# Kernel tuning notes

Hardware: AMD Instinct MI355X
Metric: run time of the kernel (lower is better)

## Reference

```python
import jax, jax.numpy as jnp
import numpy as np

B, S, E, H = 2, 2048, 512, 8
HD = E // H  # head dim = 64


def setup_inputs() -> dict:
    key = jax.random.key(0)
    k1, k2, k3 = jax.random.split(key, 3)
    scale_qkv = (6.0 / (E + 3 * E)) ** 0.5  # xavier-uniform-like scale
    scale_o = (6.0 / (E + E)) ** 0.5
    return {
        "X": jax.random.normal(k1, (B, S, E), dtype=jnp.float32),
        "Wqkv": jax.random.uniform(k2, (E, 3 * E), jnp.float32, -scale_qkv, scale_qkv),
        "bqkv": jnp.zeros((3 * E,), jnp.float32),
        "Wo": jax.random.uniform(k3, (E, E), jnp.float32, -scale_o, scale_o),
        "bo": jnp.zeros((E,), jnp.float32),
    }


def reference(X, Wqkv, bqkv, Wo, bo):
    b, s, e = X.shape
    # qkv projection: [B,S,3E] -> [B,S,H,3*HD] -> [B,H,S,3*HD]
    qkv = X @ Wqkv + bqkv
    qkv = qkv.reshape(b, s, H, 3 * HD).transpose(0, 2, 1, 3)
    q, k, v = jnp.array_split(qkv, 3, axis=-1)  # each [B,H,S,HD]
    # naive scaled dot-product attention (full score matrix, per source)
    attn_logits = jnp.einsum("bhqd,bhkd->bhqk", q, k) / jnp.sqrt(jnp.float32(HD))
    attention = jax.nn.softmax(attn_logits, axis=-1)  # [B,H,S,S]
    values = jnp.einsum("bhqk,bhkd->bhqd", attention, v)
    values = values.transpose(0, 2, 1, 3).reshape(b, s, e)
    o = values @ Wo + bo
    return (o, attention)
```

## Files before the change

### kernel.cpp

```cpp
#include <hip/hip_runtime.h>

typedef unsigned short u16;
typedef u16 u16x2 __attribute__((ext_vector_type(2)));
typedef u16 u16x4 __attribute__((ext_vector_type(4)));
typedef u16 u16x8 __attribute__((ext_vector_type(8)));
typedef __bf16 bf16x8 __attribute__((ext_vector_type(8)));
typedef float f32x4 __attribute__((ext_vector_type(4)));
typedef float f32x2 __attribute__((ext_vector_type(2)));

#define MFMA16(A, B, C) __builtin_amdgcn_mfma_f32_16x16x32_bf16(A, B, C, 0, 0, 0)

#define SB 2
#define SS 2048
#define SE 512
#define SH 8
#define SHD 64

__device__ __forceinline__ u16 f2b(float f) {
  union { float f; unsigned u; } v;
  v.f = f;
  unsigned r = v.u + 0x7FFFu + ((v.u >> 16) & 1u);
  return (u16)(r >> 16);
}

__device__ __forceinline__ bf16x8 as_bf16x8(u16x8 v) {
  return __builtin_bit_cast(bf16x8, v);
}

__global__ __launch_bounds__(256)
void prep_kernel(const float* __restrict__ X, u16* __restrict__ Xb,
                 const float* __restrict__ Wqkv, u16* __restrict__ WqkvT)
{
  __shared__ float t[32][33];
  const int tid = threadIdx.x;
  if (blockIdx.x < 2048) {
    const int i = (blockIdx.x * 256 + tid) * 4;
    const float4 v = *(const float4*)&X[i];
    u16x4 o;
    o[0] = f2b(v.x); o[1] = f2b(v.y); o[2] = f2b(v.z); o[3] = f2b(v.w);
    *(u16x4*)&Xb[i] = o;
  } else {
    const int bx = blockIdx.x - 2048;
    const int n0 = (bx % 48) * 32, k0 = (bx / 48) * 32;
    const int r = tid >> 3, c4 = (tid & 7) * 4;
    const float4 v = *(const float4*)&Wqkv[(size_t)(k0 + r) * 1536 + n0 + c4];
    t[r][c4 + 0] = v.x; t[r][c4 + 1] = v.y; t[r][c4 + 2] = v.z; t[r][c4 + 3] = v.w;
    __syncthreads();
    u16x4 o;
    o[0] = f2b(t[c4 + 0][r]);
    o[1] = f2b(t[c4 + 1][r]);
    o[2] = f2b(t[c4 + 2][r]);
    o[3] = f2b(t[c4 + 3][r]);
    *(u16x4*)&WqkvT[(n0 + r) * 512 + k0 + c4] = o;
  }
}

__global__ __launch_bounds__(256)
void wtrans_kernel(const float* __restrict__ in, u16* __restrict__ out, int N)
{
  __shared__ float t[32][33];
  const int tid = threadIdx.x;
  const int r = tid >> 3, c4 = (tid & 7) * 4;
  const int k0 = blockIdx.y * 32, n0 = blockIdx.x * 32;
  const float4 v = *(const float4*)&in[(size_t)(k0 + r) * N + n0 + c4];
  t[r][c4 + 0] = v.x; t[r][c4 + 1] = v.y; t[r][c4 + 2] = v.z; t[r][c4 + 3] = v.w;
  __syncthreads();
  u16x4 o;
  o[0] = f2b(t[c4 + 0][r]);
  o[1] = f2b(t[c4 + 1][r]);
  o[2] = f2b(t[c4 + 2][r]);
  o[3] = f2b(t[c4 + 3][r]);
  *(u16x4*)&out[(n0 + r) * 512 + k0 + c4] = o;
}

template <int MODE>
__global__ __launch_bounds__(256, 2)
void gemm_kernel(const u16* __restrict__ A, const u16* __restrict__ Bt,
                 const float* __restrict__ bias,
                 u16* __restrict__ Q, u16* __restrict__ K, u16* __restrict__ Vt,
                 float* __restrict__ Out)
{
  __shared__ __align__(16) u16 As[128 * 40];
  __shared__ __align__(16) u16 Bs[128 * 40];
  const int tid  = threadIdx.x;
  const int lane = tid & 63, wave = tid >> 6, quad = lane >> 4, l16 = lane & 15;
  const int m0 = blockIdx.y * 128, n0 = blockIdx.x * 128;
  const int wr = (wave >> 1) * 64, wc = (wave & 1) * 64;
  const int sr = tid >> 2, sc = (tid & 3) * 8;

  const f32x4 z4 = {0.f, 0.f, 0.f, 0.f};
  f32x4 acc[4][4];
#pragma unroll
  for (int i = 0; i < 4; i++)
#pragma unroll
    for (int j = 0; j < 4; j++) acc[i][j] = z4;

  for (int k0 = 0; k0 < 512; k0 += 32) {
    const u16x8 a0 = *(const u16x8*)&A[(m0 + sr) * 512 + k0 + sc];
    const u16x8 a1 = *(const u16x8*)&A[(m0 + 64 + sr) * 512 + k0 + sc];
    const u16x8 b0 = *(const u16x8*)&Bt[(n0 + sr) * 512 + k0 + sc];
    const u16x8 b1 = *(const u16x8*)&Bt[(n0 + 64 + sr) * 512 + k0 + sc];
    __syncthreads();
    *(u16x8*)&As[sr * 40 + sc]        = a0;
    *(u16x8*)&As[(64 + sr) * 40 + sc] = a1;
    *(u16x8*)&Bs[sr * 40 + sc]        = b0;
    *(u16x8*)&Bs[(64 + sr) * 40 + sc] = b1;
    __syncthreads();
    bf16x8 af[4], bf[4];
#pragma unroll
    for (int i = 0; i < 4; i++) {
      af[i] = as_bf16x8(*(const u16x8*)&As[(wr + i * 16 + l16) * 40 + quad * 8]);
      bf[i] = as_bf16x8(*(const u16x8*)&Bs[(wc + i * 16 + l16) * 40 + quad * 8]);
    }
#pragma unroll
    for (int i = 0; i < 4; i++)
#pragma unroll
      for (int j = 0; j < 4; j++) acc[i][j] = MFMA16(af[i], bf[j], acc[i][j]);
  }

#pragma unroll
  for (int tm = 0; tm < 4; tm++) {
#pragma unroll
    for (int tn = 0; tn < 4; tn++) {
#pragma unroll
      for (int r = 0; r < 4; r++) {
        const int gm = m0 + wr + tm * 16 + quad * 4 + r;
        const int gn = n0 + wc + tn * 16 + l16;
        const float v = acc[tm][tn][r] + bias[gn];
        if (MODE == 0) {
          const int bb = gm >> 11, s = gm & 2047;
          const int hh = gn / 192, j = gn - hh * 192;
          const int bh = bb * SH + hh;
          if (j < 64)
            Q[(bh * SS + s) * SHD + j] = f2b(v * 0.125f);
          else if (j < 128)
            K[(bh * SS + s) * SHD + (j - 64)] = f2b(v);
          else
            Vt[(bh * SHD + (j - 128)) * SS + s] = f2b(v);
        } else {
          Out[gm * 512 + gn] = v;
        }
      }
    }
  }
}

#define PSTR 264
#define PWAVE (16 * PSTR)

__global__ __launch_bounds__(512, 4)
void attn_kernel(const u16* __restrict__ Q, const u16* __restrict__ K,
                 const u16* __restrict__ Vt, u16* __restrict__ values,
                 float* __restrict__ attn)
{
  __shared__ __align__(16) u16 p_lds[8 * PWAVE];
  __shared__ float srm[8][16];
  __shared__ float srl[8][16];

  const int tid  = threadIdx.x;
  const int lane = tid & 63, wave = tid >> 6, quad = lane >> 4, l16 = lane & 15;
  const int q0 = blockIdx.x * 16;
  const int h = blockIdx.y, b = blockIdx.z, bh = b * SH + h;

  const u16* Qb = Q + (size_t)bh * SS * SHD;
  const u16* Kb = K + (size_t)bh * SS * SHD;
  const u16* Vb = Vt + (size_t)bh * SHD * SS;

  const bf16x8 aq0 = as_bf16x8(*(const u16x8*)&Qb[(q0 + l16) * SHD + quad * 8]);
  const bf16x8 aq1 = as_bf16x8(*(const u16x8*)&Qb[(q0 + l16) * SHD + 32 + quad * 8]);

  f32x4 acc[16];
#pragma unroll
  for (int ct = 0; ct < 16; ct++) {
    const int kb = wave * 256 + ct * 16;
    bf16x8 bk0 = as_bf16x8(*(const u16x8*)&Kb[(kb + l16) * SHD + quad * 8]);
    bf16x8 bk1 = as_bf16x8(*(const u16x8*)&Kb[(kb + l16) * SHD + 32 + quad * 8]);
    f32x4 c = {0.f, 0.f, 0.f, 0.f};
    c = MFMA16(aq0, bk0, c);
    c = MFMA16(aq1, bk1, c);
    acc[ct] = c;
  }

  float mw[4], lw[4];
#pragma unroll
  for (int r = 0; r < 4; r++) {
    float m = acc[0][r];
#pragma unroll
    for (int ct = 1; ct < 16; ct++) m = fmaxf(m, acc[ct][r]);
#pragma unroll
    for (int off = 1; off < 16; off <<= 1) m = fmaxf(m, __shfl_xor(m, off));
    mw[r] = m;
  }
#pragma unroll
  for (int r = 0; r < 4; r++) {
    float s = 0.f;
#pragma unroll
    for (int ct = 0; ct < 16; ct++) {
      const float p = __expf(acc[ct][r] - mw[r]);
      acc[ct][r] = p;
      s += p;
    }
#pragma unroll
    for (int off = 1; off < 16; off <<= 1) s += __shfl_xor(s, off);
    lw[r] = s;
  }
  if (l16 == 0) {
#pragma unroll
    for (int r = 0; r < 4; r++) {
      srm[wave][quad * 4 + r] = mw[r];
      srl[wave][quad * 4 + r] = lw[r];
    }
  }
  __syncthreads();

  float scale[4];
#pragma unroll
  for (int r = 0; r < 4; r++) {
    const int row = quad * 4 + r;
    float mg = srm[0][row];
#pragma unroll
    for (int w = 1; w < 8; w++) mg = fmaxf(mg, srm[w][row]);
    float lg = 0.f;
#pragma unroll
    for (int w = 0; w < 8; w++) lg += srl[w][row] * __expf(srm[w][row] - mg);
    scale[r] = __expf(mw[r] - mg) / lg;
  }
#pragma unroll
  for (int ct = 0; ct < 16; ct++)
#pragma unroll
    for (int r = 0; r < 4; r++) acc[ct][r] *= scale[r];

  u16* pl = &p_lds[wave * PWAVE];
#pragma unroll
  for (int ct = 0; ct < 16; ct++)
#pragma unroll
    for (int r = 0; r < 4; r++)
      pl[(quad * 4 + r) * PSTR + ct * 16 + l16] = f2b(acc[ct][r]);

  f32x4 oacc[4];
#pragma unroll
  for (int nt = 0; nt < 4; nt++) oacc[nt] = (f32x4){0.f, 0.f, 0.f, 0.f};
  bf16x8 vbuf[2][4];
  {
    const int sb = wave * 256 + quad * 8;
#pragma unroll
    for (int nt = 0; nt < 4; nt++)
      vbuf[0][nt] = as_bf16x8(*(const u16x8*)&Vb[(nt * 16 + l16) * SS + sb]);
  }
#pragma unroll
  for (int kc = 0; kc < 8; kc++) {
    if (kc < 7) {
      const int sb = wave * 256 + (kc + 1) * 32 + quad * 8;
#pragma unroll
      for (int nt = 0; nt < 4; nt++)
        vbuf[(kc + 1) & 1][nt] =
            as_bf16x8(*(const u16x8*)&Vb[(nt * 16 + l16) * SS + sb]);
    }
    bf16x8 pa = as_bf16x8(*(const u16x8*)&pl[l16 * PSTR + kc * 32 + quad * 8]);
#pragma unroll
    for (int nt = 0; nt < 4; nt++)
      oacc[nt] = MFMA16(pa, vbuf[kc & 1][nt], oacc[nt]);
  }

  float* op = (float*)pl;
#pragma unroll
  for (int nt = 0; nt < 4; nt++)
#pragma unroll
    for (int r = 0; r < 4; r++)
      op[(quad * 4 + r) * 64 + nt * 16 + l16] = oacc[nt][r];
  __syncthreads();

  const int q = tid >> 5, d0 = (tid & 31) * 2;
  f32x2 s2 = {0.f, 0.f};
#pragma unroll
  for (int w = 0; w < 8; w++) {
    const float* opw = (const float*)&p_lds[w * PWAVE];
    s2 += *(const f32x2*)&opw[q * 64 + d0];
  }
  u16x2 o2;
  o2[0] = f2b(s2[0]);
  o2[1] = f2b(s2[1]);
  *(u16x2*)&values[((size_t)(b * SS + q0 + q) * SH + h) * SHD + d0] = o2;

  float* attn_b = attn + ((size_t)bh * SS + q0) * SS;
#pragma unroll
  for (int ct = 0; ct < 16; ct++) {
    const int col = wave * 256 + ct * 16 + l16;
#pragma unroll
    for (int r = 0; r < 4; r++)
      __builtin_nontemporal_store(acc[ct][r], &attn_b[(quad * 4 + r) * SS + col]);
  }
}

extern "C" void kernel_launch(void* const* d_in, const int* in_sizes, int n_in,
                              void* d_out, int out_size, void* d_ws, size_t ws_size,
                              hipStream_t stream) {
  const float* X    = (const float*)d_in[0];
  const float* Wqkv = (const float*)d_in[1];
  const float* bqkv = (const float*)d_in[2];
  const float* Wo   = (const float*)d_in[3];
  const float* bo   = (const float*)d_in[4];

  float* o_out    = (float*)d_out;
  float* attn_out = o_out + SB * SS * SE;

  const size_t QKV_ELEMS = (size_t)SB * SH * SS * SHD;
  u16* Q      = (u16*)d_ws;
  u16* K      = Q + QKV_ELEMS;
  u16* Vt     = K + QKV_ELEMS;
  u16* values = Vt + QKV_ELEMS;
  u16* Xb     = values;
  u16* WqkvT  = (u16*)attn_out;
  u16* WoT    = Q;

  prep_kernel<<<dim3(2816), 256, 0, stream>>>(X, Xb, Wqkv, WqkvT);

  gemm_kernel<0><<<dim3(12, 32), 256, 0, stream>>>(Xb, WqkvT, bqkv, Q, K, Vt, nullptr);
  attn_kernel<<<dim3(128, 8, 2), 512, 0, stream>>>(Q, K, Vt, values, attn_out);
  wtrans_kernel<<<dim3(16, 16), 256, 0, stream>>>(Wo, WoT, 512);
  gemm_kernel<1><<<dim3(4, 32), 256, 0, stream>>>(values, WoT, bo,
                                                  nullptr, nullptr, nullptr, o_out);
}
```

Measured before the change: 421.3 us.

## Transpose MFMA operands so each lane owns one query row for vector stores

Swaps the A/B operands of the QK^T and PV MFMAs so the accumulator layout is transposed: each lane holds four consecutive key columns of a single query row. Row max and sum reductions become in-register work plus two cross-quad shuffles instead of four 16-lane shuffle trees. The attention-probability store to global memory becomes a 16-byte vector nontemporal store rather than four scalar stores, and the P and O LDS writes become vector stores, with a padded stride for O. The float-to-bf16 conversion now uses the compiler's native cast instead of manual rounding.

After: 436.8 us. 1.04x slower.

```diff
diff --git a/kernel.cpp b/kernel.cpp
--- a/kernel.cpp
+++ b/kernel.cpp
@@ -17,10 +17,7 @@
 #define SHD 64
 
 __device__ __forceinline__ u16 f2b(float f) {
-  union { float f; unsigned u; } v;
-  v.f = f;
-  unsigned r = v.u + 0x7FFFu + ((v.u >> 16) & 1u);
-  return (u16)(r >> 16);
+  return __builtin_bit_cast(u16, (__bf16)f);
 }
 
 __device__ __forceinline__ bf16x8 as_bf16x8(u16x8 v) {
@@ -147,6 +144,7 @@
 
 #define PSTR 264
 #define PWAVE (16 * PSTR)
+#define OSTR 72
 
 __global__ __launch_bounds__(512, 4)
 void attn_kernel(const u16* __restrict__ Q, const u16* __restrict__ K,
@@ -176,66 +174,59 @@
     bf16x8 bk0 = as_bf16x8(*(const u16x8*)&Kb[(kb + l16) * SHD + quad * 8]);
     bf16x8 bk1 = as_bf16x8(*(const u16x8*)&Kb[(kb + l16) * SHD + 32 + quad * 8]);
     f32x4 c = {0.f, 0.f, 0.f, 0.f};
-    c = MFMA16(aq0, bk0, c);
-    c = MFMA16(aq1, bk1, c);
+    c = MFMA16(bk0, aq0, c);
+    c = MFMA16(bk1, aq1, c);
     acc[ct] = c;
   }
 
-  float mw[4], lw[4];
-#pragma unroll
-  for (int r = 0; r < 4; r++) {
-    float m = acc[0][r];
-#pragma unroll
-    for (int ct = 1; ct < 16; ct++) m = fmaxf(m, acc[ct][r]);
-#pragma unroll
-    for (int off = 1; off < 16; off <<= 1) m = fmaxf(m, __shfl_xor(m, off));
-    mw[r] = m;
-  }
-#pragma unroll
-  for (int r = 0; r < 4; r++) {
-    float s = 0.f;
-#pragma unroll
-    for (int ct = 0; ct < 16; ct++) {
-      const float p = __expf(acc[ct][r] - mw[r]);
+  f32x4 mx4 = acc[0];
+#pragma unroll
+  for (int ct = 1; ct < 16; ct++)
+#pragma unroll
+    for (int r = 0; r < 4; r++) mx4[r] = fmaxf(mx4[r], acc[ct][r]);
+  float m = fmaxf(fmaxf(mx4[0], mx4[1]), fmaxf(mx4[2], mx4[3]));
+  m = fmaxf(m, __shfl_xor(m, 16));
+  m = fmaxf(m, __shfl_xor(m, 32));
+
+  f32x4 s4 = {0.f, 0.f, 0.f, 0.f};
+#pragma unroll
+  for (int ct = 0; ct < 16; ct++)
+#pragma unroll
+    for (int r = 0; r < 4; r++) {
+      const float p = __expf(acc[ct][r] - m);
       acc[ct][r] = p;
-      s += p;
+      s4[r] += p;
     }
-#pragma unroll
-    for (int off = 1; off < 16; off <<= 1) s += __shfl_xor(s, off);
-    lw[r] = s;
-  }
-  if (l16 == 0) {
-#pragma unroll
-    for (int r = 0; r < 4; r++) {
-      srm[wave][quad * 4 + r] = mw[r];
-      srl[wave][quad * 4 + r] = lw[r];
-    }
+  float s = (s4[0] + s4[1]) + (s4[2] + s4[3]);
+  s += __shfl_xor(s, 16);
+  s += __shfl_xor(s, 32);
+
+  if (lane < 16) {
+    srm[wave][l16] = m;
+    srl[wave][l16] = s;
   }
   __syncthreads();
 
-  float scale[4];
-#pragma unroll
-  for (int r = 0; r < 4; r++) {
-    const int row = quad * 4 + r;
-    float mg = srm[0][row];
-#pragma unroll
-    for (int w = 1; w < 8; w++) mg = fmaxf(mg, srm[w][row]);
-    float lg = 0.f;
-#pragma unroll
-    for (int w = 0; w < 8; w++) lg += srl[w][row] * __expf(srm[w][row] - mg);
-    scale[r] = __expf(mw[r] - mg) / lg;
-  }
+  float mg = srm[0][l16];
+#pragma unroll
+  for (int w = 1; w < 8; w++) mg = fmaxf(mg, srm[w][l16]);
+  float lg = 0.f;
+#pragma unroll
+  for (int w = 0; w < 8; w++) lg += srl[w][l16] * __expf(srm[w][l16] - mg);
+  const float scale = __expf(m - mg) / lg;
 #pragma unroll
   for (int ct = 0; ct < 16; ct++)
 #pragma unroll
-    for (int r = 0; r < 4; r++) acc[ct][r] *= scale[r];
+    for (int r = 0; r < 4; r++) acc[ct][r] *= scale;
 
   u16* pl = &p_lds[wave * PWAVE];
 #pragma unroll
-  for (int ct = 0; ct < 16; ct++)
-#pragma unroll
-    for (int r = 0; r < 4; r++)
-      pl[(quad * 4 + r) * PSTR + ct * 16 + l16] = f2b(acc[ct][r]);
+  for (int ct = 0; ct < 16; ct++) {
+    u16x4 t;
+#pragma unroll
+    for (int r = 0; r < 4; r++) t[r] = f2b(acc[ct][r]);
+    *(u16x4*)&pl[l16 * PSTR + ct * 16 + quad * 4] = t;
+  }
 
   f32x4 oacc[4];
 #pragma unroll
@@ -259,15 +250,13 @@
     bf16x8 pa = as_bf16x8(*(const u16x8*)&pl[l16 * PSTR + kc * 32 + quad * 8]);
 #pragma unroll
     for (int nt = 0; nt < 4; nt++)
-      oacc[nt] = MFMA16(pa, vbuf[kc & 1][nt], oacc[nt]);
+      oacc[nt] = MFMA16(vbuf[kc & 1][nt], pa, oacc[nt]);
   }
 
   float* op = (float*)pl;
 #pragma unroll
   for (int nt = 0; nt < 4; nt++)
-#pragma unroll
-    for (int r = 0; r < 4; r++)
-      op[(quad * 4 + r) * 64 + nt * 16 + l16] = oacc[nt][r];
+    *(f32x4*)&op[l16 * OSTR + nt * 16 + quad * 4] = oacc[nt];
   __syncthreads();
 
   const int q = tid >> 5, d0 = (tid & 31) * 2;
@@ -275,7 +264,7 @@
 #pragma unroll
   for (int w = 0; w < 8; w++) {
     const float* opw = (const float*)&p_lds[w * PWAVE];
-    s2 += *(const f32x2*)&opw[q * 64 + d0];
+    s2 += *(const f32x2*)&opw[q * OSTR + d0];
   }
   u16x2 o2;
   o2[0] = f2b(s2[0]);
@@ -285,10 +274,9 @@
   float* attn_b = attn + ((size_t)bh * SS + q0) * SS;
 #pragma unroll
   for (int ct = 0; ct < 16; ct++) {
-    const int col = wave * 256 + ct * 16 + l16;
-#pragma unroll
-    for (int r = 0; r < 4; r++)
-      __builtin_nontemporal_store(acc[ct][r], &attn_b[(quad * 4 + r) * SS + col]);
+    __builtin_nontemporal_store(
+        acc[ct],
+        (f32x4*)&attn_b[l16 * SS + wave * 256 + ct * 16 + quad * 4]);
   }
 }
 
```
